# Kernel optimization log

Measured on AMD Instinct MI355X. Metric: run time of the kernel, lower is better.

The kernel has to match this reference:

```python
import jax, jax.numpy as jnp
import numpy as np

B, L, C_IN = 16, 512, 32
D_MODEL, D_STATE, D_CONV, EXPAND, PRED_LEN = 128, 16, 4, 2, 96
D_INNER = EXPAND * D_MODEL          # 256
DT_RANK = (D_MODEL + 15) // 16      # 8 (ceil(d_model/16), mamba_ssm default)


def setup_inputs() -> dict:
    key = jax.random.key(0)
    ks = jax.random.split(key, 14)
    f32 = jnp.float32
    nrm = lambda k, shape, sc: jax.random.normal(k, shape, f32) * sc
    inp = {
        "x": jax.random.normal(ks[0], (B, L, C_IN), f32),
        # input_proj: Linear(enc_in, d_model)
        "W_in": nrm(ks[1], (C_IN, D_MODEL), C_IN ** -0.5),
        "b_in": jnp.zeros((D_MODEL,), f32),
        # Mamba in_proj: Linear(d_model, 2*d_inner, bias=False)
        "W_inproj": nrm(ks[2], (D_MODEL, 2 * D_INNER), D_MODEL ** -0.5),
        # depthwise causal conv1d (d_inner, d_conv) + bias
        "conv_w": nrm(ks[3], (D_INNER, D_CONV), D_CONV ** -0.5),
        "conv_b": jnp.zeros((D_INNER,), f32),
        # x_proj: Linear(d_inner, dt_rank + 2*d_state, bias=False)
        "W_xproj": nrm(ks[4], (D_INNER, DT_RANK + 2 * D_STATE), D_INNER ** -0.5),
        # dt_proj: Linear(dt_rank, d_inner) with bias init so softplus(bias) ~ 1e-3..1e-1
        "W_dt": nrm(ks[5], (DT_RANK, D_INNER), DT_RANK ** -0.5),
        "b_dt": jax.random.uniform(ks[6], (D_INNER,), f32, minval=-6.0, maxval=-3.0),
        # S4D-real A init: A = -exp(A_log), A_log = log(1..d_state)
        "A_log": jnp.log(jnp.tile(jnp.arange(1, D_STATE + 1, dtype=f32), (D_INNER, 1))),
        "D": jnp.ones((D_INNER,), f32),
        # Mamba out_proj: Linear(d_inner, d_model, bias=False)
        "W_out": nrm(ks[7], (D_INNER, D_MODEL), D_INNER ** -0.5),
        # output_proj: Linear(d_model*seq_len, pred_len*enc_in)
        "W_outproj": nrm(ks[8], (D_MODEL * L, PRED_LEN * C_IN), (D_MODEL * L) ** -0.5),
        "b_outproj": jnp.zeros((PRED_LEN * C_IN,), f32),
    }
    return inp


def _mamba_forward(x, W_in, b_in, W_inproj, conv_w, conv_b, W_xproj,
                   W_dt, b_dt, A_log, D, W_out, W_outproj, b_outproj):
    Bb, Ll, Cc = x.shape
    d_inner, d_conv = conv_w.shape
    d_state = A_log.shape[1]
    dt_rank = W_dt.shape[0]

    h = x @ W_in + b_in                                  # (B,L,d_model)
    xz = h @ W_inproj                                    # (B,L,2*d_inner)
    u, z = jnp.split(xz, 2, axis=-1)                     # each (B,L,d_inner)

    # causal depthwise conv1d along L
    uc = jnp.transpose(u, (0, 2, 1))                     # (B,d_inner,L)
    kern = conv_w[:, None, :]                            # (d_inner,1,d_conv)
    uc = jax.lax.conv_general_dilated(
        uc, kern, window_strides=(1,), padding=[(d_conv - 1, 0)],
        dimension_numbers=("NCH", "OIH", "NCH"), feature_group_count=d_inner)
    u = jax.nn.silu(jnp.transpose(uc, (0, 2, 1)) + conv_b)   # (B,L,d_inner)

    # input-dependent dt, B, C
    xdbc = u @ W_xproj                                   # (B,L,dt_rank+2*d_state)
    dt = jax.nn.softplus(xdbc[..., :dt_rank] @ W_dt + b_dt)  # (B,L,d_inner)
    Bm = xdbc[..., dt_rank:dt_rank + d_state]            # (B,L,d_state)
    Cm = xdbc[..., dt_rank + d_state:]                   # (B,L,d_state)

    A = -jnp.exp(A_log)                                  # (d_inner,d_state)
    dA = jnp.exp(jnp.einsum('bld,dn->bldn', dt, A))      # discretized A
    dBu = jnp.einsum('bld,bln,bld->bldn', dt, Bm, u)     # discretized B*u

    def step(hstate, inputs):
        dA_t, dBu_t, C_t = inputs                        # (B,d,n),(B,d,n),(B,n)
        hstate = dA_t * hstate + dBu_t
        y_t = jnp.einsum('bdn,bn->bd', hstate, C_t)
        return hstate, y_t

    h0 = jnp.zeros((Bb, d_inner, d_state), u.dtype)
    _, ys = jax.lax.scan(step, h0, (jnp.moveaxis(dA, 1, 0),
                                    jnp.moveaxis(dBu, 1, 0),
                                    jnp.moveaxis(Cm, 1, 0)))
    y = jnp.moveaxis(ys, 0, 1) + u * D                   # (B,L,d_inner)
    y = y * jax.nn.silu(z)                               # gating
    m_out = y @ W_out                                    # (B,L,d_model)

    flat = m_out.reshape(Bb, -1)                         # (B, L*d_model)
    pred = flat @ W_outproj + b_outproj                  # (B, pred_len*enc_in)
    return pred.reshape(Bb, W_outproj.shape[1] // Cc, Cc)


def reference(x, W_in, b_in, W_inproj, conv_w, conv_b, W_xproj,
              W_dt, b_dt, A_log, D, W_out, W_outproj, b_outproj):
    return _mamba_forward(x, W_in, b_in, W_inproj, conv_w, conv_b, W_xproj,
                          W_dt, b_dt, A_log, D, W_out, W_outproj, b_outproj)
```

## Files before the change

kernel.cpp:

```cpp
#include <hip/hip_runtime.h>
#include <math.h>

#define NB 16
#define LL 512
#define CIN 32
#define DM 128
#define DS 16
#define DI 256
#define DTR 8
#define NCOL 3072
#define KTOT 65536
#define ROWS 8192
#define CH 64
#define CLEN 8
#define KC 512
#define KS 128
#define OUTSZ 49152

typedef float f32x2 __attribute__((ext_vector_type(2)));

__device__ __forceinline__ float fexp_(float x){ return __expf(x); }
__device__ __forceinline__ float sigmoidf_(float x){
  return __builtin_amdgcn_rcpf(1.f + __expf(-x));
}
__device__ __forceinline__ float softplusf_(float x){
  return (x > 20.f) ? x : __logf(1.f + __expf(x));
}

__global__ void __launch_bounds__(256) k_mega1(
    const float* __restrict__ x, const float* __restrict__ W_in,
    const float* __restrict__ b_in, const float* __restrict__ W_ip,
    const float* __restrict__ cw, const float* __restrict__ cb,
    const float* __restrict__ W_xp, const float* __restrict__ Wdt,
    const float* __restrict__ bdt, const float* __restrict__ A_log,
    float* __restrict__ u, float* __restrict__ z,
    float* __restrict__ xdbc, float* __restrict__ Hc, float* __restrict__ Sdt) {
  __shared__ float xs[11][32];
  __shared__ float hs[11][128];
  __shared__ float up[11][256];
  __shared__ float ul[CLEN][256];
  __shared__ float xl[CLEN][40];
  int t = threadIdx.x;
  int b  = blockIdx.x >> 6;
  int lt = blockIdx.x & 63;
  int l0 = lt * 8;
  int row0 = (b<<9) + l0;
  for (int i=t; i<11*32; i+=256) {
    int r = i >> 5, c = i & 31;
    int li = l0 - 3 + r;
    xs[r][c] = (li >= 0) ? x[((b<<9)+li)*CIN + c] : 0.f;
  }
  __syncthreads();
  for (int i=t; i<11*128; i+=256) {
    int r = i >> 7, c = i & 127;
    float acc = b_in[c];
    #pragma unroll
    for (int k=0;k<CIN;k++) acc = fmaf(xs[r][k], W_in[k*DM+c], acc);
    hs[r][c] = acc;
  }
  __syncthreads();
  {
    int c0 = (t & 63)*4;
    int r0 = (t >> 6)*3;
    bool has2 = (r0+2 < 11);
    float acc[3][4] = {};
    for (int k4=0;k4<32;k4++) {
      float4 h0v = *(const float4*)&hs[r0][k4*4];
      float4 h1v = *(const float4*)&hs[r0+1][k4*4];
      float4 h2v = has2 ? *(const float4*)&hs[r0+2][k4*4] : make_float4(0.f,0.f,0.f,0.f);
      float h0a[4]={h0v.x,h0v.y,h0v.z,h0v.w};
      float h1a[4]={h1v.x,h1v.y,h1v.z,h1v.w};
      float h2a[4]={h2v.x,h2v.y,h2v.z,h2v.w};
      #pragma unroll
      for (int j=0;j<4;j++) {
        float4 w = *(const float4*)(W_ip + (k4*4+j)*512 + c0);
        acc[0][0]=fmaf(h0a[j],w.x,acc[0][0]); acc[0][1]=fmaf(h0a[j],w.y,acc[0][1]);
        acc[0][2]=fmaf(h0a[j],w.z,acc[0][2]); acc[0][3]=fmaf(h0a[j],w.w,acc[0][3]);
        acc[1][0]=fmaf(h1a[j],w.x,acc[1][0]); acc[1][1]=fmaf(h1a[j],w.y,acc[1][1]);
        acc[1][2]=fmaf(h1a[j],w.z,acc[1][2]); acc[1][3]=fmaf(h1a[j],w.w,acc[1][3]);
        acc[2][0]=fmaf(h2a[j],w.x,acc[2][0]); acc[2][1]=fmaf(h2a[j],w.y,acc[2][1]);
        acc[2][2]=fmaf(h2a[j],w.z,acc[2][2]); acc[2][3]=fmaf(h2a[j],w.w,acc[2][3]);
      }
    }
    *(float4*)&up[r0  ][c0] = make_float4(acc[0][0],acc[0][1],acc[0][2],acc[0][3]);
    *(float4*)&up[r0+1][c0] = make_float4(acc[1][0],acc[1][1],acc[1][2],acc[1][3]);
    if (has2)
      *(float4*)&up[r0+2][c0] = make_float4(acc[2][0],acc[2][1],acc[2][2],acc[2][3]);
  }
  {
    int c0 = (t & 63)*4;
    int r0 = (t >> 6)*2;
    float acc[2][4] = {};
    for (int k4=0;k4<32;k4++) {
      float4 h0v = *(const float4*)&hs[3+r0][k4*4];
      float4 h1v = *(const float4*)&hs[3+r0+1][k4*4];
      float h0a[4]={h0v.x,h0v.y,h0v.z,h0v.w};
      float h1a[4]={h1v.x,h1v.y,h1v.z,h1v.w};
      #pragma unroll
      for (int j=0;j<4;j++) {
        float4 w = *(const float4*)(W_ip + (k4*4+j)*512 + 256 + c0);
        acc[0][0]=fmaf(h0a[j],w.x,acc[0][0]); acc[0][1]=fmaf(h0a[j],w.y,acc[0][1]);
        acc[0][2]=fmaf(h0a[j],w.z,acc[0][2]); acc[0][3]=fmaf(h0a[j],w.w,acc[0][3]);
        acc[1][0]=fmaf(h1a[j],w.x,acc[1][0]); acc[1][1]=fmaf(h1a[j],w.y,acc[1][1]);
        acc[1][2]=fmaf(h1a[j],w.z,acc[1][2]); acc[1][3]=fmaf(h1a[j],w.w,acc[1][3]);
      }
    }
    #pragma unroll
    for (int i=0;i<2;i++) {
      int gr = row0 + r0 + i;
      *(float4*)(z + gr*DI + c0) =
        make_float4(acc[i][0],acc[i][1],acc[i][2],acc[i][3]);
    }
  }
  __syncthreads();
  for (int i=t; i<8*256; i+=256) {
    int r = i >> 8, d = i & 255;
    float s = cb[d];
    #pragma unroll
    for (int j=0;j<4;j++) {
      int li = l0 + r - 3 + j;
      if (li >= 0) s = fmaf(cw[d*4+j], up[r+j][d], s);
    }
    float uv = s * sigmoidf_(s);
    ul[r][d] = uv;
    u[(row0+r)*DI + d] = uv;
  }
  __syncthreads();
  for (int i=t; i<CLEN*40; i+=256) {
    int r = i / 40, cc = i - r*40;
    float acc = 0.f;
    #pragma unroll 8
    for (int k4=0;k4<64;k4++) {
      float4 uv = *(const float4*)&ul[r][k4*4];
      acc = fmaf(uv.x, W_xp[(k4*4+0)*40+cc], acc);
      acc = fmaf(uv.y, W_xp[(k4*4+1)*40+cc], acc);
      acc = fmaf(uv.z, W_xp[(k4*4+2)*40+cc], acc);
      acc = fmaf(uv.w, W_xp[(k4*4+3)*40+cc], acc);
    }
    xl[r][cc] = acc;
    xdbc[row0*40 + i] = acc;
  }
  __syncthreads();
  {
    int d = t, c = lt;
    float A[16], hsv[16];
    #pragma unroll
    for (int n=0;n<16;n++){ A[n] = -fexp_(A_log[d*16+n]); hsv[n]=0.f; }
    float wdt[DTR];
    #pragma unroll
    for (int j=0;j<DTR;j++) wdt[j] = Wdt[j*DI+d];
    float bdtv = bdt[d];
    float sdt = 0.f;
    for (int l=0;l<CLEN;++l) {
      float acc = bdtv;
      #pragma unroll
      for (int j=0;j<DTR;j++) acc = fmaf(xl[l][j], wdt[j], acc);
      float dtv = softplusf_(acc);
      sdt += dtv;
      float du = dtv * ul[l][d];
      #pragma unroll
      for (int n=0;n<16;n++) {
        float a = fexp_(dtv*A[n]);
        hsv[n] = fmaf(a, hsv[n], du * xl[l][DTR+n]);
      }
    }
    int hbase = ((b*CH + c)*DS)*DI + d;
    #pragma unroll
    for (int n=0;n<16;n++) Hc[hbase + n*DI] = hsv[n];
    Sdt[(b*CH + c)*DI + d] = sdt;
  }
}

__global__ void k_scan2(const float* __restrict__ A_log, const float* __restrict__ Hc,
                        const float* __restrict__ Sdt, float* __restrict__ Hst) {
  int d = threadIdx.x;
  int b = blockIdx.x >> 4, n = blockIdx.x & 15;
  float A = -fexp_(A_log[d*16+n]);
  float hs = 0.f;
  for (int c=0;c<CH;c++) {
    int off = ((b*CH + c)*DS + n)*DI + d;
    Hst[off] = hs;
    float sdt = Sdt[(b*CH + c)*DI + d];
    hs = fmaf(fexp_(A*sdt), hs, Hc[off]);
  }
}

__global__ void __launch_bounds__(256) k_scan3(
    const float* __restrict__ u, const float* __restrict__ z,
    const float* __restrict__ xdbc, const float* __restrict__ Wdt,
    const float* __restrict__ bdt, const float* __restrict__ A_log,
    const float* __restrict__ Dp, const float* __restrict__ Hst,
    const float* __restrict__ W_out, float* __restrict__ mo) {
  __shared__ float ym[CLEN][256];
  __shared__ float xl[CLEN][40];
  int t = threadIdx.x;
  int b = blockIdx.x >> 6, c = blockIdx.x & 63, d = t;
  int l0 = c * CLEN;
  int row0 = (b<<9) + l0;
  for (int i=t; i<CLEN*40; i+=256) xl[i/40][i%40] = xdbc[row0*40 + i];
  __syncthreads();
  int hbase = ((b*CH + c)*DS)*DI + d;
  float A[16], hsv[16];
  #pragma unroll
  for (int n=0;n<16;n++){ A[n] = -fexp_(A_log[d*16+n]); hsv[n] = Hst[hbase + n*DI]; }
  float wdt[DTR];
  #pragma unroll
  for (int j=0;j<DTR;j++) wdt[j] = Wdt[j*DI+d];
  float bdtv = bdt[d];
  float Dv = Dp[d];
  for (int l=0;l<CLEN;++l) {
    int row = row0 + l;
    float acc = bdtv;
    #pragma unroll
    for (int j=0;j<DTR;j++) acc = fmaf(xl[l][j], wdt[j], acc);
    float dtv = softplusf_(acc);
    float uv = u[(row<<8) + d];
    float zv = z[(row<<8) + d];
    float du = dtv * uv;
    float y = 0.f;
    #pragma unroll
    for (int n=0;n<16;n++) {
      float a = fexp_(dtv*A[n]);
      hsv[n] = fmaf(a, hsv[n], du * xl[l][DTR+n]);
      y = fmaf(hsv[n], xl[l][DTR+DS+n], y);
    }
    y = fmaf(uv, Dv, y);
    ym[l][d] = y * (zv * sigmoidf_(zv));
  }
  __syncthreads();
  int cc = t & 127;
  int rg = (t >> 7) * 4;
  float acc[4] = {};
  for (int k4=0;k4<64;k4++) {
    float w0 = W_out[(k4*4+0)*DM+cc];
    float w1 = W_out[(k4*4+1)*DM+cc];
    float w2 = W_out[(k4*4+2)*DM+cc];
    float w3 = W_out[(k4*4+3)*DM+cc];
    #pragma unroll
    for (int o=0;o<4;o++) {
      float4 yv = *(const float4*)&ym[rg+o][k4*4];
      acc[o] = fmaf(yv.w, w3, fmaf(yv.z, w2, fmaf(yv.y, w1, fmaf(yv.x, w0, acc[o]))));
    }
  }
  #pragma unroll
  for (int o=0;o<4;o++) mo[(row0+rg+o)*DM + cc] = acc[o];
}

__global__ void __launch_bounds__(256) k_final(
    const float* __restrict__ flat, const float* __restrict__ W,
    float* __restrict__ part) {
  __shared__ float lds[KC][16];
  int t = threadIdx.x;
  int n0 = blockIdx.x * 512;
  int k0 = blockIdx.y * KC;
  for (int i = t; i < 16*(KC/4); i += 256) {
    int bb  = i & 15;
    int kk4 = i >> 4;
    float4 v = *(const float4*)(flat + bb*KTOT + k0 + kk4*4);
    lds[kk4*4+0][bb] = v.x; lds[kk4*4+1][bb] = v.y;
    lds[kk4*4+2][bb] = v.z; lds[kk4*4+3][bb] = v.w;
  }
  __syncthreads();
  int c0 = n0 + t*2;
  float2 acc[16];
  #pragma unroll
  for (int b=0;b<16;b++) acc[b] = make_float2(0.f,0.f);
  const float* Wp = W + (size_t)k0*NCOL + c0;
  for (int kk=0; kk<KC; kk+=4) {
    f32x2 w0 = __builtin_nontemporal_load((const f32x2*)(Wp + (size_t)(kk+0)*NCOL));
    f32x2 w1 = __builtin_nontemporal_load((const f32x2*)(Wp + (size_t)(kk+1)*NCOL));
    f32x2 w2 = __builtin_nontemporal_load((const f32x2*)(Wp + (size_t)(kk+2)*NCOL));
    f32x2 w3 = __builtin_nontemporal_load((const f32x2*)(Wp + (size_t)(kk+3)*NCOL));
    const float4* f0 = (const float4*)&lds[kk+0][0];
    const float4* f1 = (const float4*)&lds[kk+1][0];
    const float4* f2 = (const float4*)&lds[kk+2][0];
    const float4* f3 = (const float4*)&lds[kk+3][0];
    #pragma unroll
    for (int q=0;q<4;q++) {
      float4 fa = f0[q], fb = f1[q], fc = f2[q], fd = f3[q];
      float fs0[4] = {fa.x,fa.y,fa.z,fa.w};
      float fs1[4] = {fb.x,fb.y,fb.z,fb.w};
      float fs2[4] = {fc.x,fc.y,fc.z,fc.w};
      float fs3[4] = {fd.x,fd.y,fd.z,fd.w};
      #pragma unroll
      for (int j=0;j<4;j++) {
        int b = q*4+j;
        acc[b].x=fmaf(fs0[j],w0.x,acc[b].x); acc[b].y=fmaf(fs0[j],w0.y,acc[b].y);
        acc[b].x=fmaf(fs1[j],w1.x,acc[b].x); acc[b].y=fmaf(fs1[j],w1.y,acc[b].y);
        acc[b].x=fmaf(fs2[j],w2.x,acc[b].x); acc[b].y=fmaf(fs2[j],w2.y,acc[b].y);
        acc[b].x=fmaf(fs3[j],w3.x,acc[b].x); acc[b].y=fmaf(fs3[j],w3.y,acc[b].y);
      }
    }
  }
  float* p = part + (size_t)blockIdx.y*OUTSZ;
  #pragma unroll
  for (int b=0;b<16;b++) {
    f32x2 v; v.x = acc[b].x; v.y = acc[b].y;
    __builtin_nontemporal_store(v, (f32x2*)(p + b*NCOL + c0));
  }
}

__global__ void k_reduce(const float* __restrict__ part, const float* __restrict__ bias,
                         float* __restrict__ out) {
  int idx = blockIdx.x*256 + threadIdx.x;
  float acc = bias[idx % NCOL];
  #pragma unroll 8
  for (int s=0;s<KS;s++)
    acc += __builtin_nontemporal_load(part + (size_t)s*OUTSZ + idx);
  out[idx] = acc;
}

extern "C" void kernel_launch(void* const* d_in, const int* in_sizes, int n_in,
                              void* d_out, int out_size, void* d_ws, size_t ws_size,
                              hipStream_t stream) {
  const float* x        = (const float*)d_in[0];
  const float* W_in     = (const float*)d_in[1];
  const float* b_in     = (const float*)d_in[2];
  const float* W_inproj = (const float*)d_in[3];
  const float* conv_w   = (const float*)d_in[4];
  const float* conv_b   = (const float*)d_in[5];
  const float* W_xproj  = (const float*)d_in[6];
  const float* W_dt     = (const float*)d_in[7];
  const float* b_dt     = (const float*)d_in[8];
  const float* A_log    = (const float*)d_in[9];
  const float* Dp       = (const float*)d_in[10];
  const float* W_out    = (const float*)d_in[11];
  const float* W_outproj= (const float*)d_in[12];
  const float* b_outproj= (const float*)d_in[13];
  float* out = (float*)d_out;
  float* ws  = (float*)d_ws;

  float* u    = ws;
  float* z    = ws + 2097152;
  float* xdbc = ws + 4194304;
  float* Hc   = ws + 4521984;
  float* Sdt  = ws + 8716288;
  float* Hst  = ws + 8978432;
  float* mo   = ws + 13172736;
  float* part = ws + 14221312;

  k_mega1 <<<1024, 256, 0, stream>>>(x, W_in, b_in, W_inproj, conv_w, conv_b,
                                     W_xproj, W_dt, b_dt, A_log,
                                     u, z, xdbc, Hc, Sdt);
  k_scan2 <<<256,  256, 0, stream>>>(A_log, Hc, Sdt, Hst);
  k_scan3 <<<1024, 256, 0, stream>>>(u, z, xdbc, W_dt, b_dt, A_log, Dp, Hst, W_out, mo);
  k_final <<<dim3(6, KS), 256, 0, stream>>>(mo, W_outproj, part);
  k_reduce<<<192,  256, 0, stream>>>(part, b_outproj, out);
}
```

Measured before the change: 249.9 us.

## Process 16 timesteps per block in mega1 with larger register-tiled in_proj

Each k_mega1 block now handles 16 sequence positions instead of 8, which halves the grid and the redundant conv-halo recompute of the input projection. The in_proj GEMM is restructured so half the threads compute the u half with 10-row register tiles and the other half compute z with 8-row tiles, giving more reuse of each W_inproj load. The chunk scan loops over two 8-step chunks per block. The cost is higher register pressure and fewer blocks, which may lower occupancy.

```diff
diff --git a/kernel.cpp b/kernel.cpp
--- a/kernel.cpp
+++ b/kernel.cpp
@@ -13,6 +13,8 @@
 #define ROWS 8192
 #define CH 64
 #define CLEN 8
+#define RB 16
+#define RS 19
 #define KC 512
 #define KS 128
 #define OUTSZ 49152
@@ -35,23 +37,23 @@
     const float* __restrict__ bdt, const float* __restrict__ A_log,
     float* __restrict__ u, float* __restrict__ z,
     float* __restrict__ xdbc, float* __restrict__ Hc, float* __restrict__ Sdt) {
-  __shared__ float xs[11][32];
-  __shared__ float hs[11][128];
-  __shared__ float up[11][256];
-  __shared__ float ul[CLEN][256];
-  __shared__ float xl[CLEN][40];
+  __shared__ float xs[RS][32];
+  __shared__ float hs[RS][128];
+  __shared__ float up[RS][256];
+  __shared__ float ul[RB][256];
+  __shared__ float xl[RB][40];
   int t = threadIdx.x;
-  int b  = blockIdx.x >> 6;
-  int lt = blockIdx.x & 63;
-  int l0 = lt * 8;
+  int b  = blockIdx.x >> 5;
+  int lt = blockIdx.x & 31;
+  int l0 = lt * RB;
   int row0 = (b<<9) + l0;
-  for (int i=t; i<11*32; i+=256) {
+  for (int i=t; i<RS*32; i+=256) {
     int r = i >> 5, c = i & 31;
     int li = l0 - 3 + r;
     xs[r][c] = (li >= 0) ? x[((b<<9)+li)*CIN + c] : 0.f;
   }
   __syncthreads();
-  for (int i=t; i<11*128; i+=256) {
+  for (int i=t; i<RS*128; i+=256) {
     int r = i >> 7, c = i & 127;
     float acc = b_in[c];
     #pragma unroll
@@ -60,60 +62,64 @@
   }
   __syncthreads();
   {
-    int c0 = (t & 63)*4;
-    int r0 = (t >> 6)*3;
-    bool has2 = (r0+2 < 11);
-    float acc[3][4] = {};
-    for (int k4=0;k4<32;k4++) {
-      float4 h0v = *(const float4*)&hs[r0][k4*4];
-      float4 h1v = *(const float4*)&hs[r0+1][k4*4];
-      float4 h2v = has2 ? *(const float4*)&hs[r0+2][k4*4] : make_float4(0.f,0.f,0.f,0.f);
-      float h0a[4]={h0v.x,h0v.y,h0v.z,h0v.w};
-      float h1a[4]={h1v.x,h1v.y,h1v.z,h1v.w};
-      float h2a[4]={h2v.x,h2v.y,h2v.z,h2v.w};
-      #pragma unroll
-      for (int j=0;j<4;j++) {
-        float4 w = *(const float4*)(W_ip + (k4*4+j)*512 + c0);
-        acc[0][0]=fmaf(h0a[j],w.x,acc[0][0]); acc[0][1]=fmaf(h0a[j],w.y,acc[0][1]);
-        acc[0][2]=fmaf(h0a[j],w.z,acc[0][2]); acc[0][3]=fmaf(h0a[j],w.w,acc[0][3]);
-        acc[1][0]=fmaf(h1a[j],w.x,acc[1][0]); acc[1][1]=fmaf(h1a[j],w.y,acc[1][1]);
-        acc[1][2]=fmaf(h1a[j],w.z,acc[1][2]); acc[1][3]=fmaf(h1a[j],w.w,acc[1][3]);
-        acc[2][0]=fmaf(h2a[j],w.x,acc[2][0]); acc[2][1]=fmaf(h2a[j],w.y,acc[2][1]);
-        acc[2][2]=fmaf(h2a[j],w.z,acc[2][2]); acc[2][3]=fmaf(h2a[j],w.w,acc[2][3]);
+    int lane = t & 127;
+    int rgrp = t >> 7;
+    int c0 = lane * 4;
+    if (c0 < 256) {
+      int r0 = rgrp * 9;
+      float acc[10][4] = {};
+      for (int k4=0;k4<32;k4++) {
+        float ha[10][4];
+        #pragma unroll
+        for (int i=0;i<10;i++) {
+          float4 v = *(const float4*)&hs[r0+i][k4*4];
+          ha[i][0]=v.x; ha[i][1]=v.y; ha[i][2]=v.z; ha[i][3]=v.w;
+        }
+        #pragma unroll
+        for (int j=0;j<4;j++) {
+          float4 w = *(const float4*)(W_ip + (k4*4+j)*512 + c0);
+          #pragma unroll
+          for (int i=0;i<10;i++) {
+            acc[i][0]=fmaf(ha[i][j],w.x,acc[i][0]);
+            acc[i][1]=fmaf(ha[i][j],w.y,acc[i][1]);
+            acc[i][2]=fmaf(ha[i][j],w.z,acc[i][2]);
+            acc[i][3]=fmaf(ha[i][j],w.w,acc[i][3]);
+          }
+        }
       }
-    }
-    *(float4*)&up[r0  ][c0] = make_float4(acc[0][0],acc[0][1],acc[0][2],acc[0][3]);
-    *(float4*)&up[r0+1][c0] = make_float4(acc[1][0],acc[1][1],acc[1][2],acc[1][3]);
-    if (has2)
-      *(float4*)&up[r0+2][c0] = make_float4(acc[2][0],acc[2][1],acc[2][2],acc[2][3]);
-  }
-  {
-    int c0 = (t & 63)*4;
-    int r0 = (t >> 6)*2;
-    float acc[2][4] = {};
-    for (int k4=0;k4<32;k4++) {
-      float4 h0v = *(const float4*)&hs[3+r0][k4*4];
-      float4 h1v = *(const float4*)&hs[3+r0+1][k4*4];
-      float h0a[4]={h0v.x,h0v.y,h0v.z,h0v.w};
-      float h1a[4]={h1v.x,h1v.y,h1v.z,h1v.w};
-      #pragma unroll
-      for (int j=0;j<4;j++) {
-        float4 w = *(const float4*)(W_ip + (k4*4+j)*512 + 256 + c0);
-        acc[0][0]=fmaf(h0a[j],w.x,acc[0][0]); acc[0][1]=fmaf(h0a[j],w.y,acc[0][1]);
-        acc[0][2]=fmaf(h0a[j],w.z,acc[0][2]); acc[0][3]=fmaf(h0a[j],w.w,acc[0][3]);
-        acc[1][0]=fmaf(h1a[j],w.x,acc[1][0]); acc[1][1]=fmaf(h1a[j],w.y,acc[1][1]);
-        acc[1][2]=fmaf(h1a[j],w.z,acc[1][2]); acc[1][3]=fmaf(h1a[j],w.w,acc[1][3]);
+      #pragma unroll
+      for (int i=0;i<10;i++)
+        *(float4*)&up[r0+i][c0] = make_float4(acc[i][0],acc[i][1],acc[i][2],acc[i][3]);
+    } else {
+      int r0z = rgrp * 8;
+      float acc[8][4] = {};
+      for (int k4=0;k4<32;k4++) {
+        float ha[8][4];
+        #pragma unroll
+        for (int i=0;i<8;i++) {
+          float4 v = *(const float4*)&hs[3+r0z+i][k4*4];
+          ha[i][0]=v.x; ha[i][1]=v.y; ha[i][2]=v.z; ha[i][3]=v.w;
+        }
+        #pragma unroll
+        for (int j=0;j<4;j++) {
+          float4 w = *(const float4*)(W_ip + (k4*4+j)*512 + c0);
+          #pragma unroll
+          for (int i=0;i<8;i++) {
+            acc[i][0]=fmaf(ha[i][j],w.x,acc[i][0]);
+            acc[i][1]=fmaf(ha[i][j],w.y,acc[i][1]);
+            acc[i][2]=fmaf(ha[i][j],w.z,acc[i][2]);
+            acc[i][3]=fmaf(ha[i][j],w.w,acc[i][3]);
+          }
+        }
       }
-    }
-    #pragma unroll
-    for (int i=0;i<2;i++) {
-      int gr = row0 + r0 + i;
-      *(float4*)(z + gr*DI + c0) =
-        make_float4(acc[i][0],acc[i][1],acc[i][2],acc[i][3]);
-    }
-  }
-  __syncthreads();
-  for (int i=t; i<8*256; i+=256) {
+      #pragma unroll
+      for (int i=0;i<8;i++)
+        *(float4*)(z + (row0+r0z+i)*DI + (c0-256)) =
+          make_float4(acc[i][0],acc[i][1],acc[i][2],acc[i][3]);
+    }
+  }
+  __syncthreads();
+  for (int i=t; i<RB*256; i+=256) {
     int r = i >> 8, d = i & 255;
     float s = cb[d];
     #pragma unroll
@@ -126,7 +132,7 @@
     u[(row0+r)*DI + d] = uv;
   }
   __syncthreads();
-  for (int i=t; i<CLEN*40; i+=256) {
+  for (int i=t; i<RB*40; i+=256) {
     int r = i / 40, cc = i - r*40;
     float acc = 0.f;
     #pragma unroll 8
@@ -142,32 +148,39 @@
   }
   __syncthreads();
   {
-    int d = t, c = lt;
-    float A[16], hsv[16];
-    #pragma unroll
-    for (int n=0;n<16;n++){ A[n] = -fexp_(A_log[d*16+n]); hsv[n]=0.f; }
+    int d = t;
+    float A[16];
+    #pragma unroll
+    for (int n=0;n<16;n++) A[n] = -fexp_(A_log[d*16+n]);
     float wdt[DTR];
     #pragma unroll
     for (int j=0;j<DTR;j++) wdt[j] = Wdt[j*DI+d];
     float bdtv = bdt[d];
-    float sdt = 0.f;
-    for (int l=0;l<CLEN;++l) {
-      float acc = bdtv;
-      #pragma unroll
-      for (int j=0;j<DTR;j++) acc = fmaf(xl[l][j], wdt[j], acc);
-      float dtv = softplusf_(acc);
-      sdt += dtv;
-      float du = dtv * ul[l][d];
-      #pragma unroll
-      for (int n=0;n<16;n++) {
-        float a = fexp_(dtv*A[n]);
-        hsv[n] = fmaf(a, hsv[n], du * xl[l][DTR+n]);
+    for (int cc=0; cc<2; ++cc) {
+      int cg = lt*2 + cc;
+      float hsv[16];
+      #pragma unroll
+      for (int n=0;n<16;n++) hsv[n] = 0.f;
+      float sdt = 0.f;
+      for (int l=0;l<CLEN;++l) {
+        int rr = cc*CLEN + l;
+        float acc = bdtv;
+        #pragma unroll
+        for (int j=0;j<DTR;j++) acc = fmaf(xl[rr][j], wdt[j], acc);
+        float dtv = softplusf_(acc);
+        sdt += dtv;
+        float du = dtv * ul[rr][d];
+        #pragma unroll
+        for (int n=0;n<16;n++) {
+          float a = fexp_(dtv*A[n]);
+          hsv[n] = fmaf(a, hsv[n], du * xl[rr][DTR+n]);
+        }
       }
-    }
-    int hbase = ((b*CH + c)*DS)*DI + d;
-    #pragma unroll
-    for (int n=0;n<16;n++) Hc[hbase + n*DI] = hsv[n];
-    Sdt[(b*CH + c)*DI + d] = sdt;
+      int hbase = ((b*CH + cg)*DS)*DI + d;
+      #pragma unroll
+      for (int n=0;n<16;n++) Hc[hbase + n*DI] = hsv[n];
+      Sdt[(b*CH + cg)*DI + d] = sdt;
+    }
   }
 }
 
@@ -339,7 +352,7 @@
   float* mo   = ws + 13172736;
   float* part = ws + 14221312;
 
-  k_mega1 <<<1024, 256, 0, stream>>>(x, W_in, b_in, W_inproj, conv_w, conv_b,
+  k_mega1 <<<512,  256, 0, stream>>>(x, W_in, b_in, W_inproj, conv_w, conv_b,
                                      W_xproj, W_dt, b_dt, A_log,
                                      u, z, xdbc, Hc, Sdt);
   k_scan2 <<<256,  256, 0, stream>>>(A_log, Hc, Sdt, Hst);
```

Measured after the change: 238.1 us. -4.7%, faster.
